# Optimization experiments

Measured on AMD Instinct MI355X. Metric: run time of the kernel, lower is better.

The kernel has to match this reference:

```python
import jax, jax.numpy as jnp
import numpy as np

HIDDEN = 1024
N_HEAD = 16
HEAD_DIM = HIDDEN // N_HEAD  # 64
BATCH = 1
SEQ = 4096
THETA = 10000.0


def _rope_cos_sin(seq_len, head_dim, dtype=jnp.float32):
    # freqs[t, j] = t / theta^(2j/dim), j in [0, dim/2)
    inv_freq = 1.0 / (THETA ** (jnp.arange(0, head_dim, 2, dtype=dtype) / head_dim))
    t = jnp.arange(seq_len, dtype=dtype)
    freqs = jnp.outer(t, inv_freq)           # [S, D/2]
    return jnp.cos(freqs), jnp.sin(freqs)


def _apply_rope(x, cos, sin):
    # x: [B, S, H, D]; pairs (x[...,2j], x[...,2j+1]) rotated by angle freqs[t, j]
    x2 = x.reshape(*x.shape[:-1], -1, 2)       # [B, S, H, D/2, 2]
    x_re, x_im = x2[..., 0], x2[..., 1]
    c = cos[None, :, None, :]                   # [1, S, 1, D/2]
    s = sin[None, :, None, :]
    out_re = x_re * c - x_im * s
    out_im = x_re * s + x_im * c
    out = jnp.stack([out_re, out_im], axis=-1)  # [B, S, H, D/2, 2]
    return out.reshape(x.shape)


def setup_inputs() -> dict:
    key = jax.random.key(0)
    kx, kq, kk, kv = jax.random.split(key, 4)
    scale = 1.0 / np.sqrt(HIDDEN)
    return {
        "x": jax.random.normal(kx, (BATCH, SEQ, HIDDEN), dtype=jnp.float32),
        "wq": jax.random.normal(kq, (HIDDEN, HIDDEN), dtype=jnp.float32) * scale,
        "wk": jax.random.normal(kk, (HIDDEN, HIDDEN), dtype=jnp.float32) * scale,
        "wv": jax.random.normal(kv, (HIDDEN, HIDDEN), dtype=jnp.float32) * scale,
    }


def reference(x, wq, wk, wv):
    B, S, _ = x.shape
    # torch nn.Linear(no bias): y = x @ W.T
    xq = (x @ wq.T).reshape(B, S, N_HEAD, HEAD_DIM).astype(jnp.float32)
    xk = (x @ wk.T).reshape(B, S, N_HEAD, HEAD_DIM).astype(jnp.float32)
    xv = (x @ wv.T).reshape(B, S, N_HEAD, HEAD_DIM).astype(jnp.float32)

    cos, sin = _rope_cos_sin(S, HEAD_DIM)
    q = _apply_rope(xq, cos, sin)
    k = _apply_rope(xk, cos, sin)

    # [B, H, S, S] scores, no causal mask (matches source)
    scores = jnp.einsum("bqhd,bkhd->bhqk", q, k) / jnp.sqrt(
        jnp.asarray(HEAD_DIM, dtype=q.dtype))
    attn = jax.nn.softmax(scores, axis=-1)
    out = jnp.einsum("bhqk,bkhd->bqhd", attn, xv)  # [B, S, H, D]
    return out.reshape(B, S, N_HEAD * HEAD_DIM)
```

## Files before the change

### kernel.cpp

```cpp
#include <hip/hip_runtime.h>
#include <stdint.h>


#define SEQLEN 4096
#define NHEAD 16
#define HDIM 64

typedef __bf16 bf16x8 __attribute__((ext_vector_type(8)));
typedef float f32x4 __attribute__((ext_vector_type(4)));
typedef float f32x16 __attribute__((ext_vector_type(16)));

__device__ __forceinline__ unsigned short f2bf(float f) {
  union { float f; unsigned int u; } v; v.f = f;
  unsigned int r = v.u + 0x7FFFu + ((v.u >> 16) & 1u);
  return (unsigned short)(r >> 16);
}
__device__ __forceinline__ unsigned int pkc(float lo, float hi) {
  union { __bf16 b[2]; unsigned int u; } z;
  z.b[0] = (__bf16)lo; z.b[1] = (__bf16)hi;
  return z.u;
}
__device__ __forceinline__ bf16x8 as_bf(uint4 v) { return __builtin_bit_cast(bf16x8, v); }
__device__ __forceinline__ f32x4 mfma16(bf16x8 a, bf16x8 b, f32x4 c) {
  return __builtin_amdgcn_mfma_f32_16x16x32_bf16(a, b, c, 0, 0, 0);
}
__device__ __forceinline__ f32x16 mfma32(bf16x8 a, bf16x8 b, f32x16 c) {
  return __builtin_amdgcn_mfma_f32_32x32x16_bf16(a, b, c, 0, 0, 0);
}

__global__ __launch_bounds__(256) void k_convert(
    const float* __restrict__ x, const float* __restrict__ wq,
    const float* __restrict__ wk, const float* __restrict__ wv,
    unsigned short* __restrict__ xbf, unsigned short* __restrict__ wbf) {
  int i = blockIdx.x * 256 + threadIdx.x;
  const int NX = SEQLEN * 1024 / 4;
  const int NW = 1024 * 1024 / 4;
  float4 v;
  unsigned short* dst;
  int di;
  if (i < NX) {
    v = ((const float4*)x)[i]; dst = xbf; di = i;
  } else {
    int j = i - NX;
    const float4* src = (const float4*)((j < NW) ? wq : (j < 2 * NW) ? wk : wv);
    v = src[j & (NW - 1)];
    dst = wbf; di = j;
  }
  ushort4 o; o.x = f2bf(v.x); o.y = f2bf(v.y); o.z = f2bf(v.z); o.w = f2bf(v.w);
  ((ushort4*)dst)[di] = o;
}

__global__ __launch_bounds__(256) void k_table(float* __restrict__ ct, float* __restrict__ st) {
  int i = blockIdx.x * 256 + threadIdx.x;
  int s = i >> 5, j = i & 31;
  double inv = exp(-(double)j * 0.28782313662425572);
  double a = (double)s * inv;
  ct[i] = (float)cos(a);
  st[i] = (float)sin(a);
}

__global__ __launch_bounds__(256) void k_gemm(
    const unsigned short* __restrict__ xbf, const unsigned short* __restrict__ wbf,
    const float* __restrict__ ct, const float* __restrict__ st,
    unsigned short* __restrict__ qbf, unsigned short* __restrict__ KF,
    unsigned short* __restrict__ VF) {
  __shared__ __align__(16) unsigned short As[2][128 * 40];
  __shared__ __align__(16) unsigned short Bs[2][128 * 40];
  const int t = threadIdx.x;
  const int bn = blockIdx.x, bm = blockIdx.y;
  const int lane = t & 63, wave = t >> 6;
  const int r = lane & 15, g = lane >> 4;
  const int wm = wave >> 1, wn = wave & 1;

  const int c0 = t, c1 = t + 256;
  const int ar0 = c0 >> 2, ao0 = (c0 & 3) * 16;
  const int ar1 = c1 >> 2, ao1 = (c1 & 3) * 16;

  const char* pA0 = (const char*)xbf + (size_t)(bm * 128 + ar0) * 2048 + ao0;
  const char* pA1 = (const char*)xbf + (size_t)(bm * 128 + ar1) * 2048 + ao1;
  const char* pB0 = (const char*)wbf + (size_t)(bn * 128 + ar0) * 2048 + ao0;
  const char* pB1 = (const char*)wbf + (size_t)(bn * 128 + ar1) * 2048 + ao1;

  uint4 ra0, ra1, rb0, rb1;
#define LD_TILE                                   \
  ra0 = *(const uint4*)pA0; ra1 = *(const uint4*)pA1; \
  rb0 = *(const uint4*)pB0; rb1 = *(const uint4*)pB1; \
  pA0 += 64; pA1 += 64; pB0 += 64; pB1 += 64;

  LD_TILE
  f32x4 zero4 = {0.f, 0.f, 0.f, 0.f};
  f32x4 acc[4][4];
#pragma unroll
  for (int m = 0; m < 4; ++m)
#pragma unroll
    for (int n = 0; n < 4; ++n) acc[m][n] = zero4;

  for (int kk = 0; kk < 32; ++kk) {
    unsigned short* Ac = As[kk & 1];
    unsigned short* Bc = Bs[kk & 1];
    *(uint4*)((char*)Ac + ar0 * 80 + ao0) = ra0;
    *(uint4*)((char*)Ac + ar1 * 80 + ao1) = ra1;
    *(uint4*)((char*)Bc + ar0 * 80 + ao0) = rb0;
    *(uint4*)((char*)Bc + ar1 * 80 + ao1) = rb1;
    __syncthreads();
    if (kk < 31) { LD_TILE }
    bf16x8 af[4], bfr[4];
#pragma unroll
    for (int m = 0; m < 4; ++m)
      af[m] = as_bf(*(const uint4*)((const char*)Ac + (wm * 64 + m * 16 + r) * 80 + g * 16));
#pragma unroll
    for (int n = 0; n < 4; ++n)
      bfr[n] = as_bf(*(const uint4*)((const char*)Bc + (wn * 64 + n * 16 + r) * 80 + g * 16));
#pragma unroll
    for (int m = 0; m < 4; ++m)
#pragma unroll
      for (int n = 0; n < 4; ++n)
        acc[m][n] = mfma16(af[m], bfr[n], acc[m][n]);
  }

  const int matid = bn >> 3;
#pragma unroll
  for (int m = 0; m < 4; ++m) {
    const int row0 = bm * 128 + wm * 64 + m * 16 + 4 * g;
#pragma unroll
    for (int n = 0; n < 4; ++n) {
      const int col = bn * 128 + wn * 64 + n * 16 + r;
      const int d = col & 63;
      const int hh = (col >> 6) & 15;
      if (matid < 2) {
        const int jdx = (col >> 1) & 31;
        const float sgn = (col & 1) ? 1.0f : -1.0f;
        const float qs = (matid == 0) ? 0.18033688011112042f : 1.0f;
        size_t kfi0 = (size_t)hh * 262144 + (size_t)(row0 >> 5) * 2048 +
                      (size_t)((d >> 4) & 3) * 512 +
                      (size_t)((((d >> 3) & 1) * 32) + (row0 & 31)) * 8 + (d & 7);
#pragma unroll
        for (int j = 0; j < 4; ++j) {
          float v = acc[m][n][j];
          float p = __shfl_xor(v, 1);
          int srow = row0 + j;
          float cv = ct[srow * 32 + jdx];
          float sv = st[srow * 32 + jdx];
          float o = (v * cv + p * sv * sgn) * qs;
          if (matid == 0) {
            qbf[(size_t)srow * 1024 + (hh * 64 + d)] = f2bf(o);
          } else {
            KF[kfi0 + (size_t)j * 8] = f2bf(o);
          }
        }
      } else {
        ushort4 o;
        o.x = f2bf(acc[m][n][0]); o.y = f2bf(acc[m][n][1]);
        o.z = f2bf(acc[m][n][2]); o.w = f2bf(acc[m][n][3]);
        const int kt = row0 >> 5, q4 = (row0 >> 2) & 7;
        const int kc = q4 >> 2, bb = (q4 >> 1) & 1, h2 = q4 & 1;
        const int dt = d >> 5, l2 = d & 31;
        size_t off = (size_t)hh * 524288 + (size_t)kt * 4096 + (size_t)dt * 2048 +
                     (size_t)kc * 1024 + (size_t)(h2 * 32 + l2) * 16 + bb * 8;
        *(ushort4*)((char*)VF + off) = o;
      }
    }
  }
}

__global__ __launch_bounds__(512) void k_attn(
    const unsigned short* __restrict__ qbf, const unsigned short* __restrict__ KF,
    const unsigned short* __restrict__ VF, float* __restrict__ out) {
  __shared__ __align__(16) char smem[33280];
  const int t = threadIdx.x;
  const int b = blockIdx.x;
  const int work = (b & 7) * 64 + (b >> 3);
  const int h = work >> 5;
  const int qb = work & 31;
  const int lane = t & 63, wave = t >> 6;
  const int qw = wave & 3, hf = wave >> 2;
  const int li = lane & 31, hi = lane >> 5;
  const int q0 = qb * 128 + qw * 32;

  bf16x8 qf[4];
#pragma unroll
  for (int c = 0; c < 4; ++c)
    qf[c] = as_bf(*(const uint4*)((const char*)qbf +
              (size_t)(q0 + li) * 2048 + h * 128 + c * 32 + hi * 16));

  f32x16 z16 = {0.f};
  f32x16 acc[2];
  acc[0] = z16; acc[1] = z16;
  float l4[4] = {0.f, 0.f, 0.f, 0.f};

  const char* pK = (const char*)KF + (size_t)h * 524288 + (size_t)hf * 262144 + lane * 16;
  const char* pV = (const char*)VF + (size_t)h * 524288 + (size_t)hf * 262144 + lane * 16;

#define LDFRAG(kb, vb)                               \
  kb##0 = *(const uint4*)(pK);                       \
  kb##1 = *(const uint4*)(pK + 1024);                \
  kb##2 = *(const uint4*)(pK + 2048);                \
  kb##3 = *(const uint4*)(pK + 3072);                \
  vb##0 = *(const uint4*)(pV);                       \
  vb##1 = *(const uint4*)(pV + 1024);                \
  vb##2 = *(const uint4*)(pV + 2048);                \
  vb##3 = *(const uint4*)(pV + 3072);                \
  pK += 4096; pV += 4096;

#define BODY(kb, vb)                                                           \
  {                                                                            \
    f32x16 sT = z16;                                                           \
    __builtin_amdgcn_s_setprio(1);                                             \
    sT = mfma32(as_bf(kb##0), qf[0], sT);                                      \
    sT = mfma32(as_bf(kb##1), qf[1], sT);                                      \
    sT = mfma32(as_bf(kb##2), qf[2], sT);                                      \
    sT = mfma32(as_bf(kb##3), qf[3], sT);                                      \
    __builtin_amdgcn_s_setprio(0);                                             \
    _Pragma("unroll")                                                          \
    for (int i = 0; i < 16; ++i) sT[i] = __builtin_amdgcn_exp2f(sT[i]);        \
    _Pragma("unroll")                                                          \
    for (int i = 0; i < 4; ++i)                                                \
      l4[i] += (sT[i] + sT[i + 4]) + (sT[i + 8] + sT[i + 12]);                 \
    uint4 bw0, bw1;                                                            \
    bw0.x = pkc(sT[0], sT[1]);  bw0.y = pkc(sT[2], sT[3]);                     \
    bw0.z = pkc(sT[4], sT[5]);  bw0.w = pkc(sT[6], sT[7]);                     \
    bw1.x = pkc(sT[8], sT[9]);  bw1.y = pkc(sT[10], sT[11]);                   \
    bw1.z = pkc(sT[12], sT[13]); bw1.w = pkc(sT[14], sT[15]);                  \
    bf16x8 p0 = as_bf(bw0), p1 = as_bf(bw1);                                   \
    __builtin_amdgcn_s_setprio(1);                                             \
    acc[0] = mfma32(as_bf(vb##0), p0, acc[0]);                                 \
    acc[1] = mfma32(as_bf(vb##2), p0, acc[1]);                                 \
    acc[0] = mfma32(as_bf(vb##1), p1, acc[0]);                                 \
    acc[1] = mfma32(as_bf(vb##3), p1, acc[1]);                                 \
    __builtin_amdgcn_s_setprio(0);                                             \
  }

  uint4 ka0, ka1, ka2, ka3, va0, va1, va2, va3;
  uint4 kb0, kb1, kb2, kb3, vb0, vb1, vb2, vb3;

  LDFRAG(ka, va)
  for (int j = 0; j < 64; j += 2) {
    LDFRAG(kb, vb)
    BODY(ka, va)
    if (j + 2 < 64) { LDFRAG(ka, va) }
    BODY(kb, vb)
  }

  float lrun = (l4[0] + l4[1]) + (l4[2] + l4[3]);
  float lhalf = lrun + __shfl_xor(lrun, 32);

  __syncthreads();
  float* shm = (float*)smem;
  if (hf == 1) {
    float* ab = shm + qw * 2048;
#pragma unroll
    for (int dt = 0; dt < 2; ++dt)
#pragma unroll
      for (int i = 0; i < 16; ++i) {
        int d = (i & 3) + 8 * (i >> 2) + 4 * hi + 32 * dt;
        ab[d * 32 + li] = acc[dt][i];
      }
    if (hi == 0) shm[8192 + qw * 32 + li] = lhalf;
  }
  __syncthreads();
  if (hf == 0) {
    float* ab = shm + qw * 2048;
    float l1 = shm[8192 + qw * 32 + li];
    float linv = 1.0f / (lhalf + l1);
#pragma unroll
    for (int dt = 0; dt < 2; ++dt)
#pragma unroll
      for (int i = 0; i < 16; ++i) {
        int d = (i & 3) + 8 * (i >> 2) + 4 * hi + 32 * dt;
        acc[dt][i] = (acc[dt][i] + ab[d * 32 + li]) * linv;
      }
    __asm__ volatile("" ::: "memory");

    float* eb = shm + qw * 2048;
#pragma unroll
    for (int dt = 0; dt < 2; ++dt) {
#pragma unroll
      for (int i = 0; i < 16; ++i)
        eb[li * 33 + ((i & 3) + 8 * (i >> 2) + 4 * hi)] = acc[dt][i];
      __asm__ volatile("" ::: "memory");
#pragma unroll
      for (int it = 0; it < 16; ++it) {
        int q = it * 2 + hi;
        float v = eb[q * 33 + li];
        out[(size_t)(q0 + q) * 1024 + h * 64 + dt * 32 + li] = v;
      }
      __asm__ volatile("" ::: "memory");
    }
  }
}

extern "C" void kernel_launch(void* const* d_in, const int* in_sizes, int n_in,
                              void* d_out, int out_size, void* d_ws, size_t ws_size,
                              hipStream_t stream) {
  const float* x  = (const float*)d_in[0];
  const float* wq = (const float*)d_in[1];
  const float* wk = (const float*)d_in[2];
  const float* wv = (const float*)d_in[3];
  float* out = (float*)d_out;
  char* ws = (char*)d_ws;

  unsigned short* qbf = (unsigned short*)(ws);
  unsigned short* KF  = (unsigned short*)(ws + ((size_t)8 << 20));
  unsigned short* VF  = (unsigned short*)(ws + ((size_t)16 << 20));
  unsigned short* xbf = (unsigned short*)(ws + ((size_t)24 << 20));
  unsigned short* wbf = (unsigned short*)(ws + ((size_t)32 << 20));
  float* ct = (float*)(ws + ((size_t)38 << 20));
  float* st = (float*)(ws + ((size_t)38 << 20) + ((size_t)512 << 10));

  k_convert<<<dim3(7168), dim3(256), 0, stream>>>(x, wq, wk, wv, xbf, wbf);
  k_table<<<dim3(512), dim3(256), 0, stream>>>(ct, st);
  k_gemm<<<dim3(24, 32), dim3(256), 0, stream>>>(xbf, wbf, ct, st, qbf, KF, VF);
  k_attn<<<dim3(512), dim3(512), 0, stream>>>(qbf, KF, VF, out);
}
```

Measured before the change: 155.0 us.

## Process two query tiles per wave to reuse K/V fragments in attention

The attention kernel now runs 4 waves per block instead of 8, and each wave handles 64 query rows (two 32-row tiles) instead of 32. Every K/V fragment loaded from global memory feeds MFMAs for both tiles, which halves K/V load traffic per query and gives more independent MFMA chains to interleave. The cost is higher register pressure (two sets of accumulators, Q fragments and score tiles), which may lower occupancy. The epilogue's shared-memory reduction and transposed store are adjusted for the new layout.

```diff
diff --git a/kernel.cpp b/kernel.cpp
--- a/kernel.cpp
+++ b/kernel.cpp
@@ -163,30 +163,33 @@
   }
 }
 
-__global__ __launch_bounds__(512) void k_attn(
+__global__ __launch_bounds__(256) void k_attn(
     const unsigned short* __restrict__ qbf, const unsigned short* __restrict__ KF,
     const unsigned short* __restrict__ VF, float* __restrict__ out) {
-  __shared__ __align__(16) char smem[33280];
+  __shared__ __align__(16) float shm[8320];
   const int t = threadIdx.x;
   const int b = blockIdx.x;
   const int work = (b & 7) * 64 + (b >> 3);
   const int h = work >> 5;
   const int qb = work & 31;
   const int lane = t & 63, wave = t >> 6;
-  const int qw = wave & 3, hf = wave >> 2;
+  const int qg = wave & 1, hf = wave >> 1;
   const int li = lane & 31, hi = lane >> 5;
-  const int q0 = qb * 128 + qw * 32;
-
-  bf16x8 qf[4];
-#pragma unroll
-  for (int c = 0; c < 4; ++c)
-    qf[c] = as_bf(*(const uint4*)((const char*)qbf +
-              (size_t)(q0 + li) * 2048 + h * 128 + c * 32 + hi * 16));
+  const int q0 = qb * 128 + qg * 64;
+
+  const char* qbase = (const char*)qbf + (size_t)(q0 + li) * 2048 + h * 128 + hi * 16;
+  bf16x8 qfA[4], qfB[4];
+#pragma unroll
+  for (int c = 0; c < 4; ++c) {
+    qfA[c] = as_bf(*(const uint4*)(qbase + c * 32));
+    qfB[c] = as_bf(*(const uint4*)(qbase + 32 * 2048 + c * 32));
+  }
 
   f32x16 z16 = {0.f};
-  f32x16 acc[2];
-  acc[0] = z16; acc[1] = z16;
-  float l4[4] = {0.f, 0.f, 0.f, 0.f};
+  f32x16 accA[2], accB[2];
+  accA[0] = z16; accA[1] = z16; accB[0] = z16; accB[1] = z16;
+  float l4A[4] = {0.f, 0.f, 0.f, 0.f};
+  float l4B[4] = {0.f, 0.f, 0.f, 0.f};
 
   const char* pK = (const char*)KF + (size_t)h * 524288 + (size_t)hf * 262144 + lane * 16;
   const char* pV = (const char*)VF + (size_t)h * 524288 + (size_t)hf * 262144 + lane * 16;
@@ -204,29 +207,45 @@
 
 #define BODY(kb, vb)                                                           \
   {                                                                            \
-    f32x16 sT = z16;                                                           \
+    f32x16 sT0 = z16, sT1 = z16;                                               \
     __builtin_amdgcn_s_setprio(1);                                             \
-    sT = mfma32(as_bf(kb##0), qf[0], sT);                                      \
-    sT = mfma32(as_bf(kb##1), qf[1], sT);                                      \
-    sT = mfma32(as_bf(kb##2), qf[2], sT);                                      \
-    sT = mfma32(as_bf(kb##3), qf[3], sT);                                      \
+    sT0 = mfma32(as_bf(kb##0), qfA[0], sT0);                                   \
+    sT1 = mfma32(as_bf(kb##0), qfB[0], sT1);                                   \
+    sT0 = mfma32(as_bf(kb##1), qfA[1], sT0);                                   \
+    sT1 = mfma32(as_bf(kb##1), qfB[1], sT1);                                   \
+    sT0 = mfma32(as_bf(kb##2), qfA[2], sT0);                                   \
+    sT1 = mfma32(as_bf(kb##2), qfB[2], sT1);                                   \
+    sT0 = mfma32(as_bf(kb##3), qfA[3], sT0);                                   \
+    sT1 = mfma32(as_bf(kb##3), qfB[3], sT1);                                   \
     __builtin_amdgcn_s_setprio(0);                                             \
     _Pragma("unroll")                                                          \
-    for (int i = 0; i < 16; ++i) sT[i] = __builtin_amdgcn_exp2f(sT[i]);        \
+    for (int i = 0; i < 16; ++i) sT0[i] = __builtin_amdgcn_exp2f(sT0[i]);      \
     _Pragma("unroll")                                                          \
-    for (int i = 0; i < 4; ++i)                                                \
-      l4[i] += (sT[i] + sT[i + 4]) + (sT[i + 8] + sT[i + 12]);                 \
-    uint4 bw0, bw1;                                                            \
-    bw0.x = pkc(sT[0], sT[1]);  bw0.y = pkc(sT[2], sT[3]);                     \
-    bw0.z = pkc(sT[4], sT[5]);  bw0.w = pkc(sT[6], sT[7]);                     \
-    bw1.x = pkc(sT[8], sT[9]);  bw1.y = pkc(sT[10], sT[11]);                   \
-    bw1.z = pkc(sT[12], sT[13]); bw1.w = pkc(sT[14], sT[15]);                  \
-    bf16x8 p0 = as_bf(bw0), p1 = as_bf(bw1);                                   \
+    for (int i = 0; i < 16; ++i) sT1[i] = __builtin_amdgcn_exp2f(sT1[i]);      \
+    _Pragma("unroll")                                                          \
+    for (int i = 0; i < 4; ++i) {                                              \
+      l4A[i] += (sT0[i] + sT0[i + 4]) + (sT0[i + 8] + sT0[i + 12]);            \
+      l4B[i] += (sT1[i] + sT1[i + 4]) + (sT1[i + 8] + sT1[i + 12]);            \
+    }                                                                          \
+    uint4 a0, a1, b0, b1;                                                      \
+    a0.x = pkc(sT0[0], sT0[1]);   a0.y = pkc(sT0[2], sT0[3]);                  \
+    a0.z = pkc(sT0[4], sT0[5]);   a0.w = pkc(sT0[6], sT0[7]);                  \
+    a1.x = pkc(sT0[8], sT0[9]);   a1.y = pkc(sT0[10], sT0[11]);                \
+    a1.z = pkc(sT0[12], sT0[13]); a1.w = pkc(sT0[14], sT0[15]);                \
+    b0.x = pkc(sT1[0], sT1[1]);   b0.y = pkc(sT1[2], sT1[3]);                  \
+    b0.z = pkc(sT1[4], sT1[5]);   b0.w = pkc(sT1[6], sT1[7]);                  \
+    b1.x = pkc(sT1[8], sT1[9]);   b1.y = pkc(sT1[10], sT1[11]);                \
+    b1.z = pkc(sT1[12], sT1[13]); b1.w = pkc(sT1[14], sT1[15]);                \
+    bf16x8 pA0 = as_bf(a0), pA1 = as_bf(a1), pB0 = as_bf(b0), pB1 = as_bf(b1); \
     __builtin_amdgcn_s_setprio(1);                                             \
-    acc[0] = mfma32(as_bf(vb##0), p0, acc[0]);                                 \
-    acc[1] = mfma32(as_bf(vb##2), p0, acc[1]);                                 \
-    acc[0] = mfma32(as_bf(vb##1), p1, acc[0]);                                 \
-    acc[1] = mfma32(as_bf(vb##3), p1, acc[1]);                                 \
+    accA[0] = mfma32(as_bf(vb##0), pA0, accA[0]);                              \
+    accA[1] = mfma32(as_bf(vb##2), pA0, accA[1]);                              \
+    accB[0] = mfma32(as_bf(vb##0), pB0, accB[0]);                              \
+    accB[1] = mfma32(as_bf(vb##2), pB0, accB[1]);                              \
+    accA[0] = mfma32(as_bf(vb##1), pA1, accA[0]);                              \
+    accA[1] = mfma32(as_bf(vb##3), pA1, accA[1]);                              \
+    accB[0] = mfma32(as_bf(vb##1), pB1, accB[0]);                              \
+    accB[1] = mfma32(as_bf(vb##3), pB1, accB[1]);                              \
     __builtin_amdgcn_s_setprio(0);                                             \
   }
 
@@ -241,45 +260,51 @@
     BODY(kb, vb)
   }
 
-  float lrun = (l4[0] + l4[1]) + (l4[2] + l4[3]);
-  float lhalf = lrun + __shfl_xor(lrun, 32);
-
+  float lrA = (l4A[0] + l4A[1]) + (l4A[2] + l4A[3]);
+  float lrB = (l4B[0] + l4B[1]) + (l4B[2] + l4B[3]);
+  float lqA = lrA + __shfl_xor(lrA, 32);
+  float lqB = lrB + __shfl_xor(lrB, 32);
+
+  float* O = shm + qg * 4096;
+  float* ST = shm + 8192;
   __syncthreads();
-  float* shm = (float*)smem;
   if (hf == 1) {
-    float* ab = shm + qw * 2048;
 #pragma unroll
     for (int dt = 0; dt < 2; ++dt)
 #pragma unroll
       for (int i = 0; i < 16; ++i) {
         int d = (i & 3) + 8 * (i >> 2) + 4 * hi + 32 * dt;
-        ab[d * 32 + li] = acc[dt][i];
-      }
-    if (hi == 0) shm[8192 + qw * 32 + li] = lhalf;
+        O[d * 64 + li] = accA[dt][i];
+        O[d * 64 + 32 + li] = accB[dt][i];
+      }
+    if (hi == 0) { ST[qg * 64 + li] = lqA; ST[qg * 64 + 32 + li] = lqB; }
   }
   __syncthreads();
   if (hf == 0) {
-    float* ab = shm + qw * 2048;
-    float l1 = shm[8192 + qw * 32 + li];
-    float linv = 1.0f / (lhalf + l1);
+    float linvA = 1.0f / (lqA + ST[qg * 64 + li]);
+    float linvB = 1.0f / (lqB + ST[qg * 64 + 32 + li]);
 #pragma unroll
     for (int dt = 0; dt < 2; ++dt)
 #pragma unroll
       for (int i = 0; i < 16; ++i) {
         int d = (i & 3) + 8 * (i >> 2) + 4 * hi + 32 * dt;
-        acc[dt][i] = (acc[dt][i] + ab[d * 32 + li]) * linv;
+        accA[dt][i] = (accA[dt][i] + O[d * 64 + li]) * linvA;
+        accB[dt][i] = (accB[dt][i] + O[d * 64 + 32 + li]) * linvB;
       }
     __asm__ volatile("" ::: "memory");
 
-    float* eb = shm + qw * 2048;
+    float* eb = O;
 #pragma unroll
     for (int dt = 0; dt < 2; ++dt) {
 #pragma unroll
-      for (int i = 0; i < 16; ++i)
-        eb[li * 33 + ((i & 3) + 8 * (i >> 2) + 4 * hi)] = acc[dt][i];
+      for (int i = 0; i < 16; ++i) {
+        int d = (i & 3) + 8 * (i >> 2) + 4 * hi;
+        eb[li * 33 + d] = accA[dt][i];
+        eb[(32 + li) * 33 + d] = accB[dt][i];
+      }
       __asm__ volatile("" ::: "memory");
 #pragma unroll
-      for (int it = 0; it < 16; ++it) {
+      for (int it = 0; it < 32; ++it) {
         int q = it * 2 + hi;
         float v = eb[q * 33 + li];
         out[(size_t)(q0 + q) * 1024 + h * 64 + dt * 32 + li] = v;
@@ -310,5 +335,5 @@
   k_convert<<<dim3(7168), dim3(256), 0, stream>>>(x, wq, wk, wv, xbf, wbf);
   k_table<<<dim3(512), dim3(256), 0, stream>>>(ct, st);
   k_gemm<<<dim3(24, 32), dim3(256), 0, stream>>>(xbf, wbf, ct, st, qbf, KF, VF);
-  k_attn<<<dim3(512), dim3(512), 0, stream>>>(qbf, KF, VF, out);
-}
+  k_attn<<<dim3(512), dim3(256), 0, stream>>>(qbf, KF, VF, out);
+}
```

After: 164.0 us. +5.8%, slower.
